# Kernel tuning notes

Measured on AMD Instinct MI355X. Metric: run time of the kernel, lower is better.

## Reference

```python
import jax, jax.numpy as jnp
import numpy as np

BATCH = 8192
N_FEATURES = 512
DEPTH = 10
N_LEAVES = 2 ** DEPTH
ATOMS = N_FEATURES + 1  # include_one=True
TAU = 1.0


def eml(a, b):
    # Assumed definition of the custom binary eml op: smooth-max / log-sum-exp.
    # eml(a, b) = log(exp(a) + exp(b)), computed stably.
    return jnp.logaddexp(a, b)


def setup_inputs() -> dict:
    key = jax.random.key(0)
    k1, k2 = jax.random.split(key)
    X = jax.random.normal(k1, (BATCH, N_FEATURES), dtype=jnp.float32)
    leaf_logits = jax.random.normal(k2, (N_LEAVES, ATOMS), dtype=jnp.float32) * 0.1
    return {"X": X, "leaf_logits": leaf_logits}


def reference(X, leaf_logits):
    batch = X.shape[0]
    # atom values: prepend constant 1 (include_one=True) -> (batch, atoms)
    atom_values = jnp.concatenate([jnp.ones((batch, 1), dtype=X.dtype), X], axis=1)
    # softmax over atoms per leaf, then mix: (batch, n_leaves)
    weights = jax.nn.softmax(leaf_logits / TAU, axis=-1)
    current = jnp.einsum('ba,la->bl', atom_values, weights)
    # binary tree reduction: log2(n_leaves) steps over strided slices
    while current.shape[-1] > 1:
        current = eml(current[..., 0::2], current[..., 1::2])
    return current.squeeze(-1)  # (batch,)
```

## Files before the change

kernel.cpp:

```cpp
#include <hip/hip_runtime.h>
#include <hip/hip_bf16.h>

#define BATCH 8192
#define NF 512
#define NL 1024
#define ATOMS 513

typedef float float4v __attribute__((ext_vector_type(4)));
typedef short short8 __attribute__((ext_vector_type(8)));

__device__ __forceinline__ unsigned short f2bf(float f) {
    union { float f; unsigned int u; } cv; cv.f = f;
    unsigned int u = cv.u;
    u += 0x7fffu + ((u >> 16) & 1u);
    return (unsigned short)(u >> 16);
}

__device__ __forceinline__ void load_lds16(const unsigned short* g, unsigned short* ldsbase) {
    __builtin_amdgcn_global_load_lds(
        (const __attribute__((address_space(1))) unsigned int*)g,
        (__attribute__((address_space(3))) unsigned int*)ldsbase,
        16, 0, 0);
}

__global__ void convert_kernel(const float* __restrict__ X,
                               unsigned short* __restrict__ Xb) {
    size_t i = ((size_t)blockIdx.x * 256 + threadIdx.x) * 8;
    float4v x0 = *reinterpret_cast<const float4v*>(X + i);
    float4v x1 = *reinterpret_cast<const float4v*>(X + i + 4);
    short8 a;
    a[0] = (short)f2bf(x0[0]); a[1] = (short)f2bf(x0[1]);
    a[2] = (short)f2bf(x0[2]); a[3] = (short)f2bf(x0[3]);
    a[4] = (short)f2bf(x1[0]); a[5] = (short)f2bf(x1[1]);
    a[6] = (short)f2bf(x1[2]); a[7] = (short)f2bf(x1[3]);
    *reinterpret_cast<short8*>(Xb + i) = a;
}

__global__ void softmax_kernel(const float* __restrict__ logits,
                               unsigned short* __restrict__ Wb,
                               float* __restrict__ bias) {
    int l = blockIdx.x;
    int t = threadIdx.x;
    int wave = t >> 6, lane = t & 63;
    const float* row = logits + (size_t)l * ATOMS;
    float v0 = row[t];
    float v1 = row[t + 256];
    float v2 = (t == 0) ? row[512] : -1e30f;

    __shared__ float red[8];
    float m = fmaxf(fmaxf(v0, v1), v2);
#pragma unroll
    for (int o = 32; o > 0; o >>= 1) m = fmaxf(m, __shfl_xor(m, o, 64));
    if (lane == 0) red[wave] = m;
    __syncthreads();
    float mx = fmaxf(fmaxf(red[0], red[1]), fmaxf(red[2], red[3]));

    float e0 = __expf(v0 - mx);
    float e1 = __expf(v1 - mx);
    float e2 = (t == 0) ? __expf(v2 - mx) : 0.f;
    float s = e0 + e1 + e2;
#pragma unroll
    for (int o = 32; o > 0; o >>= 1) s += __shfl_xor(s, o, 64);
    if (lane == 0) red[4 + wave] = s;
    __syncthreads();
    float inv = 1.f / (red[4] + red[5] + red[6] + red[7]);

    unsigned short* wrow = Wb + (size_t)l * NF;
    if (t == 0) {
        bias[l] = e0 * inv;
        wrow[511] = f2bf(e2 * inv);
    } else {
        wrow[t - 1] = f2bf(e0 * inv);
    }
    wrow[t + 255] = f2bf(e1 * inv);
}

__global__ __launch_bounds__(256, 2)
void gemm_lse_kernel(const unsigned short* __restrict__ Xb,
                     const unsigned short* __restrict__ Wb,
                     const float* __restrict__ bias,
                     float* __restrict__ partial) {
    __shared__ unsigned short As[128 * 32];
    __shared__ unsigned short Bs[128 * 32];
    __shared__ float sums[2][128];

    int tid  = threadIdx.x;
    int wave = tid >> 6;
    int lane = tid & 63;
    int quad = lane >> 4;
    int l16  = lane & 15;
    int wr = wave >> 1;
    int wc = wave & 1;

    int mb = blockIdx.x >> 3;
    int nb = blockIdx.x & 7;
    int R0 = mb * 128;
    int N0 = nb * 128;

    int srow = wave * 32 + (lane >> 2);
    int selem = (lane & 3) * 8;

    float4v acc[4][4];
#pragma unroll
    for (int mt = 0; mt < 4; ++mt)
#pragma unroll
        for (int nt = 0; nt < 4; ++nt)
            acc[mt][nt] = (float4v){0.f, 0.f, 0.f, 0.f};

    for (int kt = 0; kt < 16; ++kt) {
        int kb = kt * 32;
        const unsigned short* ga = Xb + (size_t)(R0 + srow) * NF + kb + selem;
        const unsigned short* gb = Wb + (size_t)(N0 + srow) * NF + kb + selem;
        load_lds16(ga,            &As[(wave * 32) * 32]);
        load_lds16(ga + 16 * NF,  &As[(wave * 32 + 16) * 32]);
        load_lds16(gb,            &Bs[(wave * 32) * 32]);
        load_lds16(gb + 16 * NF,  &Bs[(wave * 32 + 16) * 32]);
        __syncthreads();

        short8 af[4], bfr[4];
#pragma unroll
        for (int mt = 0; mt < 4; ++mt)
            af[mt] = *reinterpret_cast<const short8*>(
                &As[(wr * 64 + mt * 16 + l16) * 32 + quad * 8]);
#pragma unroll
        for (int nt = 0; nt < 4; ++nt)
            bfr[nt] = *reinterpret_cast<const short8*>(
                &Bs[(wc * 64 + nt * 16 + l16) * 32 + quad * 8]);

#pragma unroll
        for (int mt = 0; mt < 4; ++mt)
#pragma unroll
            for (int nt = 0; nt < 4; ++nt)
                acc[mt][nt] = __builtin_amdgcn_mfma_f32_16x16x32_bf16(
                    af[mt], bfr[nt], acc[mt][nt], 0, 0, 0);
        __syncthreads();
    }

    float ps[4][4];
#pragma unroll
    for (int mt = 0; mt < 4; ++mt)
#pragma unroll
        for (int r = 0; r < 4; ++r) ps[mt][r] = 0.f;

#pragma unroll
    for (int nt = 0; nt < 4; ++nt) {
        float bl = bias[N0 + wc * 64 + nt * 16 + l16];
#pragma unroll
        for (int mt = 0; mt < 4; ++mt)
#pragma unroll
            for (int r = 0; r < 4; ++r)
                ps[mt][r] += __expf(acc[mt][nt][r] + bl);
    }

#pragma unroll
    for (int m = 1; m < 16; m <<= 1)
#pragma unroll
        for (int mt = 0; mt < 4; ++mt)
#pragma unroll
            for (int r = 0; r < 4; ++r)
                ps[mt][r] += __shfl_xor(ps[mt][r], m, 64);

    if (l16 == 0) {
#pragma unroll
        for (int mt = 0; mt < 4; ++mt)
#pragma unroll
            for (int r = 0; r < 4; ++r)
                sums[wc][wr * 64 + mt * 16 + quad * 4 + r] = ps[mt][r];
    }
    __syncthreads();
    if (tid < 128)
        partial[(size_t)nb * BATCH + R0 + tid] = sums[0][tid] + sums[1][tid];
}

__global__ void combine_kernel(const float* __restrict__ partial,
                               float* __restrict__ out) {
    int i = blockIdx.x * 256 + threadIdx.x;
    float s = 0.f;
#pragma unroll
    for (int c = 0; c < 8; ++c) s += partial[(size_t)c * BATCH + i];
    out[i] = logf(s);
}

extern "C" void kernel_launch(void* const* d_in, const int* in_sizes, int n_in,
                              void* d_out, int out_size, void* d_ws, size_t ws_size,
                              hipStream_t stream) {
    const float* X      = (const float*)d_in[0];
    const float* logits = (const float*)d_in[1];
    float* out = (float*)d_out;

    char* ws = (char*)d_ws;
    unsigned short* Xb   = (unsigned short*)ws;
    unsigned short* Wb   = (unsigned short*)(ws + (size_t)BATCH * NF * 2);
    float*          bias = (float*)(ws + (size_t)BATCH * NF * 2 + (size_t)NL * NF * 2);
    float*          part = (float*)(ws + (size_t)BATCH * NF * 2 + (size_t)NL * NF * 2 + NL * 4);

    convert_kernel<<<(BATCH * NF) / (256 * 8), 256, 0, stream>>>(X, Xb);
    softmax_kernel<<<NL, 256, 0, stream>>>(logits, Wb, bias);
    gemm_lse_kernel<<<(BATCH / 128) * (NL / 128), 256, 0, stream>>>(Xb, Wb, bias, part);
    combine_kernel<<<BATCH / 256, 256, 0, stream>>>(part, out);
}
```

Before: 86.73 us.

## Merge prep kernels and fold combine into GEMM via atomics with last-block finalize

Merges the bf16 convert and softmax kernels into one prep launch that also zeroes the accumulators, and removes the combine kernel. GEMM blocks now atomically add their partial sum-exp into a per-row buffer, and the last block per row tile (found with a counter) applies the log. The block index mapping also changes so row tiles vary fastest, and the loop address math is hoisted. This cuts two launches and a global round trip, at the cost of atomics, a thread fence and float summation order that is no longer deterministic.

```diff
diff --git a/kernel.cpp b/kernel.cpp
--- a/kernel.cpp
+++ b/kernel.cpp
@@ -23,66 +23,84 @@
         16, 0, 0);
 }
 
-__global__ void convert_kernel(const float* __restrict__ X,
-                               unsigned short* __restrict__ Xb) {
-    size_t i = ((size_t)blockIdx.x * 256 + threadIdx.x) * 8;
-    float4v x0 = *reinterpret_cast<const float4v*>(X + i);
-    float4v x1 = *reinterpret_cast<const float4v*>(X + i + 4);
-    short8 a;
-    a[0] = (short)f2bf(x0[0]); a[1] = (short)f2bf(x0[1]);
-    a[2] = (short)f2bf(x0[2]); a[3] = (short)f2bf(x0[3]);
-    a[4] = (short)f2bf(x1[0]); a[5] = (short)f2bf(x1[1]);
-    a[6] = (short)f2bf(x1[2]); a[7] = (short)f2bf(x1[3]);
-    *reinterpret_cast<short8*>(Xb + i) = a;
-}
-
-__global__ void softmax_kernel(const float* __restrict__ logits,
-                               unsigned short* __restrict__ Wb,
-                               float* __restrict__ bias) {
-    int l = blockIdx.x;
-    int t = threadIdx.x;
-    int wave = t >> 6, lane = t & 63;
-    const float* row = logits + (size_t)l * ATOMS;
-    float v0 = row[t];
-    float v1 = row[t + 256];
-    float v2 = (t == 0) ? row[512] : -1e30f;
-
-    __shared__ float red[8];
-    float m = fmaxf(fmaxf(v0, v1), v2);
-#pragma unroll
-    for (int o = 32; o > 0; o >>= 1) m = fmaxf(m, __shfl_xor(m, o, 64));
-    if (lane == 0) red[wave] = m;
-    __syncthreads();
-    float mx = fmaxf(fmaxf(red[0], red[1]), fmaxf(red[2], red[3]));
-
-    float e0 = __expf(v0 - mx);
-    float e1 = __expf(v1 - mx);
-    float e2 = (t == 0) ? __expf(v2 - mx) : 0.f;
-    float s = e0 + e1 + e2;
-#pragma unroll
-    for (int o = 32; o > 0; o >>= 1) s += __shfl_xor(s, o, 64);
-    if (lane == 0) red[4 + wave] = s;
-    __syncthreads();
-    float inv = 1.f / (red[4] + red[5] + red[6] + red[7]);
-
-    unsigned short* wrow = Wb + (size_t)l * NF;
-    if (t == 0) {
-        bias[l] = e0 * inv;
-        wrow[511] = f2bf(e2 * inv);
-    } else {
-        wrow[t - 1] = f2bf(e0 * inv);
-    }
-    wrow[t + 255] = f2bf(e1 * inv);
+#define N_CONVERT_BLOCKS 2048
+#define N_SOFTMAX_BLOCKS 1024
+#define N_ZERO_BLOCKS    33
+
+__global__ void prep_kernel(const float* __restrict__ X,
+                            const float* __restrict__ logits,
+                            unsigned short* __restrict__ Xb,
+                            unsigned short* __restrict__ Wb,
+                            float* __restrict__ bias,
+                            float* __restrict__ sumexp,
+                            int* __restrict__ cnt) {
+    int bi = blockIdx.x;
+    int t  = threadIdx.x;
+
+    if (bi < N_CONVERT_BLOCKS) {
+        size_t i = ((size_t)bi * 256 + t) * 8;
+        float4v x0 = *reinterpret_cast<const float4v*>(X + i);
+        float4v x1 = *reinterpret_cast<const float4v*>(X + i + 4);
+        short8 a;
+        a[0] = (short)f2bf(x0[0]); a[1] = (short)f2bf(x0[1]);
+        a[2] = (short)f2bf(x0[2]); a[3] = (short)f2bf(x0[3]);
+        a[4] = (short)f2bf(x1[0]); a[5] = (short)f2bf(x1[1]);
+        a[6] = (short)f2bf(x1[2]); a[7] = (short)f2bf(x1[3]);
+        *reinterpret_cast<short8*>(Xb + i) = a;
+        return;
+    }
+    if (bi < N_CONVERT_BLOCKS + N_SOFTMAX_BLOCKS) {
+        int l = bi - N_CONVERT_BLOCKS;
+        int wave = t >> 6, lane = t & 63;
+        const float* row = logits + (size_t)l * ATOMS;
+        float v0 = row[t];
+        float v1 = row[t + 256];
+        float v2 = (t == 0) ? row[512] : -1e30f;
+
+        __shared__ float red[8];
+        float m = fmaxf(fmaxf(v0, v1), v2);
+#pragma unroll
+        for (int o = 32; o > 0; o >>= 1) m = fmaxf(m, __shfl_xor(m, o, 64));
+        if (lane == 0) red[wave] = m;
+        __syncthreads();
+        float mx = fmaxf(fmaxf(red[0], red[1]), fmaxf(red[2], red[3]));
+
+        float e0 = __expf(v0 - mx);
+        float e1 = __expf(v1 - mx);
+        float e2 = (t == 0) ? __expf(v2 - mx) : 0.f;
+        float s = e0 + e1 + e2;
+#pragma unroll
+        for (int o = 32; o > 0; o >>= 1) s += __shfl_xor(s, o, 64);
+        if (lane == 0) red[4 + wave] = s;
+        __syncthreads();
+        float inv = 1.f / (red[4] + red[5] + red[6] + red[7]);
+
+        unsigned short* wrow = Wb + (size_t)l * NF;
+        if (t == 0) {
+            bias[l] = e0 * inv;
+            wrow[511] = f2bf(e2 * inv);
+        } else {
+            wrow[t - 1] = f2bf(e0 * inv);
+        }
+        wrow[t + 255] = f2bf(e1 * inv);
+        return;
+    }
+    int i = (bi - N_CONVERT_BLOCKS - N_SOFTMAX_BLOCKS) * 256 + t;
+    if (i < BATCH) sumexp[i] = 0.f;
+    else { int j = i - BATCH; if (j < 64) cnt[j] = 0; }
 }
 
 __global__ __launch_bounds__(256, 2)
 void gemm_lse_kernel(const unsigned short* __restrict__ Xb,
                      const unsigned short* __restrict__ Wb,
                      const float* __restrict__ bias,
-                     float* __restrict__ partial) {
+                     float* __restrict__ sumexp,
+                     int* __restrict__ cnt,
+                     float* __restrict__ out) {
     __shared__ unsigned short As[128 * 32];
     __shared__ unsigned short Bs[128 * 32];
     __shared__ float sums[2][128];
+    __shared__ int lastFlag;
 
     int tid  = threadIdx.x;
     int wave = tid >> 6;
@@ -92,13 +110,27 @@
     int wr = wave >> 1;
     int wc = wave & 1;
 
-    int mb = blockIdx.x >> 3;
-    int nb = blockIdx.x & 7;
+    int mb = blockIdx.x & 63;
+    int nb = blockIdx.x >> 6;
     int R0 = mb * 128;
     int N0 = nb * 128;
 
-    int srow = wave * 32 + (lane >> 2);
+    int srow  = wave * 32 + (lane >> 2);
     int selem = (lane & 3) * 8;
+    const unsigned short* ga = Xb + (size_t)(R0 + srow) * NF + selem;
+    const unsigned short* gb = Wb + (size_t)(N0 + srow) * NF + selem;
+    unsigned short* la0 = &As[(wave * 32) * 32];
+    unsigned short* la1 = &As[(wave * 32 + 16) * 32];
+    unsigned short* lb0 = &Bs[(wave * 32) * 32];
+    unsigned short* lb1 = &Bs[(wave * 32 + 16) * 32];
+
+    const unsigned short* pa = &As[(wr * 64 + l16) * 32 + quad * 8];
+    const unsigned short* pb = &Bs[(wc * 64 + l16) * 32 + quad * 8];
+
+    float bl[4];
+#pragma unroll
+    for (int nt = 0; nt < 4; ++nt)
+        bl[nt] = bias[N0 + wc * 64 + nt * 16 + l16];
 
     float4v acc[4][4];
 #pragma unroll
@@ -108,24 +140,20 @@
             acc[mt][nt] = (float4v){0.f, 0.f, 0.f, 0.f};
 
     for (int kt = 0; kt < 16; ++kt) {
-        int kb = kt * 32;
-        const unsigned short* ga = Xb + (size_t)(R0 + srow) * NF + kb + selem;
-        const unsigned short* gb = Wb + (size_t)(N0 + srow) * NF + kb + selem;
-        load_lds16(ga,            &As[(wave * 32) * 32]);
-        load_lds16(ga + 16 * NF,  &As[(wave * 32 + 16) * 32]);
-        load_lds16(gb,            &Bs[(wave * 32) * 32]);
-        load_lds16(gb + 16 * NF,  &Bs[(wave * 32 + 16) * 32]);
+        load_lds16(ga,           la0);
+        load_lds16(ga + 16 * NF, la1);
+        load_lds16(gb,           lb0);
+        load_lds16(gb + 16 * NF, lb1);
+        ga += 32; gb += 32;
         __syncthreads();
 
         short8 af[4], bfr[4];
 #pragma unroll
         for (int mt = 0; mt < 4; ++mt)
-            af[mt] = *reinterpret_cast<const short8*>(
-                &As[(wr * 64 + mt * 16 + l16) * 32 + quad * 8]);
+            af[mt] = *reinterpret_cast<const short8*>(pa + mt * 16 * 32);
 #pragma unroll
         for (int nt = 0; nt < 4; ++nt)
-            bfr[nt] = *reinterpret_cast<const short8*>(
-                &Bs[(wc * 64 + nt * 16 + l16) * 32 + quad * 8]);
+            bfr[nt] = *reinterpret_cast<const short8*>(pb + nt * 16 * 32);
 
 #pragma unroll
         for (int mt = 0; mt < 4; ++mt)
@@ -143,14 +171,12 @@
         for (int r = 0; r < 4; ++r) ps[mt][r] = 0.f;
 
 #pragma unroll
-    for (int nt = 0; nt < 4; ++nt) {
-        float bl = bias[N0 + wc * 64 + nt * 16 + l16];
+    for (int nt = 0; nt < 4; ++nt)
 #pragma unroll
         for (int mt = 0; mt < 4; ++mt)
 #pragma unroll
             for (int r = 0; r < 4; ++r)
-                ps[mt][r] += __expf(acc[mt][nt][r] + bl);
-    }
+                ps[mt][r] += __expf(acc[mt][nt][r] + bl[nt]);
 
 #pragma unroll
     for (int m = 1; m < 16; m <<= 1)
@@ -168,17 +194,23 @@
                 sums[wc][wr * 64 + mt * 16 + quad * 4 + r] = ps[mt][r];
     }
     __syncthreads();
+
     if (tid < 128)
-        partial[(size_t)nb * BATCH + R0 + tid] = sums[0][tid] + sums[1][tid];
-}
-
-__global__ void combine_kernel(const float* __restrict__ partial,
-                               float* __restrict__ out) {
-    int i = blockIdx.x * 256 + threadIdx.x;
-    float s = 0.f;
-#pragma unroll
-    for (int c = 0; c < 8; ++c) s += partial[(size_t)c * BATCH + i];
-    out[i] = logf(s);
+        atomicAdd(&sumexp[R0 + tid], sums[0][tid] + sums[1][tid]);
+
+    __threadfence();
+    __syncthreads();
+    if (tid == 0) {
+        int old = __hip_atomic_fetch_add(&cnt[mb], 1, __ATOMIC_ACQ_REL,
+                                         __HIP_MEMORY_SCOPE_AGENT);
+        lastFlag = (old == 7);
+    }
+    __syncthreads();
+    if (lastFlag && tid < 128) {
+        float s = __hip_atomic_load(&sumexp[R0 + tid], __ATOMIC_RELAXED,
+                                    __HIP_MEMORY_SCOPE_AGENT);
+        out[R0 + tid] = logf(s);
+    }
 }
 
 extern "C" void kernel_launch(void* const* d_in, const int* in_sizes, int n_in,
@@ -191,11 +223,12 @@
     char* ws = (char*)d_ws;
     unsigned short* Xb   = (unsigned short*)ws;
     unsigned short* Wb   = (unsigned short*)(ws + (size_t)BATCH * NF * 2);
-    float*          bias = (float*)(ws + (size_t)BATCH * NF * 2 + (size_t)NL * NF * 2);
-    float*          part = (float*)(ws + (size_t)BATCH * NF * 2 + (size_t)NL * NF * 2 + NL * 4);
-
-    convert_kernel<<<(BATCH * NF) / (256 * 8), 256, 0, stream>>>(X, Xb);
-    softmax_kernel<<<NL, 256, 0, stream>>>(logits, Wb, bias);
-    gemm_lse_kernel<<<(BATCH / 128) * (NL / 128), 256, 0, stream>>>(Xb, Wb, bias, part);
-    combine_kernel<<<BATCH / 256, 256, 0, stream>>>(part, out);
-}
+    float* bias   = (float*)(ws + (size_t)BATCH * NF * 2 + (size_t)NL * NF * 2);
+    float* sumexp = (float*)((char*)bias + NL * sizeof(float));
+    int*   cnt    = (int*)((char*)sumexp + BATCH * sizeof(float));
+
+    prep_kernel<<<N_CONVERT_BLOCKS + N_SOFTMAX_BLOCKS + N_ZERO_BLOCKS, 256, 0, stream>>>(
+        X, logits, Xb, Wb, bias, sumexp, cnt);
+    gemm_lse_kernel<<<(BATCH / 128) * (NL / 128), 256, 0, stream>>>(
+        Xb, Wb, bias, sumexp, cnt, out);
+}
```

Result: slower. 116.3 us (+34.1%).

## Double-buffer LDS tiles in GEMM to prefetch next K-slice during MFMA

Applied to the files above, without the earlier changes.

The GEMM kernel gets two LDS buffers for the A and B tiles. The first K-slice is loaded before the loop, and each iteration issues the async global-to-LDS loads for the next slice before running the MFMAs on the current one. This hides global load latency behind compute and leaves one barrier per iteration instead of two. The costs are double the LDS per block (about 32KB), which could limit occupancy, and a redundant duplicate fragment-load loop that the compiler should eliminate.

```diff
diff --git a/kernel.cpp b/kernel.cpp
--- a/kernel.cpp
+++ b/kernel.cpp
@@ -80,8 +80,8 @@
                      const unsigned short* __restrict__ Wb,
                      const float* __restrict__ bias,
                      float* __restrict__ partial) {
-    __shared__ unsigned short As[128 * 32];
-    __shared__ unsigned short Bs[128 * 32];
+    __shared__ unsigned short As[2][128 * 32];
+    __shared__ unsigned short Bs[2][128 * 32];
     __shared__ float sums[2][128];
 
     int tid  = threadIdx.x;
@@ -97,8 +97,10 @@
     int R0 = mb * 128;
     int N0 = nb * 128;
 
-    int srow = wave * 32 + (lane >> 2);
+    int srow  = wave * 32 + (lane >> 2);
     int selem = (lane & 3) * 8;
+    const unsigned short* ga = Xb + (size_t)(R0 + srow) * NF + selem;
+    const unsigned short* gb = Wb + (size_t)(N0 + srow) * NF + selem;
 
     float4v acc[4][4];
 #pragma unroll
@@ -107,25 +109,41 @@
         for (int nt = 0; nt < 4; ++nt)
             acc[mt][nt] = (float4v){0.f, 0.f, 0.f, 0.f};
 
+    {
+        load_lds16(ga,           &As[0][(wave * 32) * 32]);
+        load_lds16(ga + 16 * NF, &As[0][(wave * 32 + 16) * 32]);
+        load_lds16(gb,           &Bs[0][(wave * 32) * 32]);
+        load_lds16(gb + 16 * NF, &Bs[0][(wave * 32 + 16) * 32]);
+    }
+    __syncthreads();
+
+    int frag_off = (wr * 64 + l16) * 32 + quad * 8;
+
     for (int kt = 0; kt < 16; ++kt) {
-        int kb = kt * 32;
-        const unsigned short* ga = Xb + (size_t)(R0 + srow) * NF + kb + selem;
-        const unsigned short* gb = Wb + (size_t)(N0 + srow) * NF + kb + selem;
-        load_lds16(ga,            &As[(wave * 32) * 32]);
-        load_lds16(ga + 16 * NF,  &As[(wave * 32 + 16) * 32]);
-        load_lds16(gb,            &Bs[(wave * 32) * 32]);
-        load_lds16(gb + 16 * NF,  &Bs[(wave * 32 + 16) * 32]);
-        __syncthreads();
+        int cur = kt & 1;
+        if (kt < 15) {
+            const unsigned short* a = ga + (kt + 1) * 32;
+            const unsigned short* b = gb + (kt + 1) * 32;
+            int nxt = cur ^ 1;
+            load_lds16(a,           &As[nxt][(wave * 32) * 32]);
+            load_lds16(a + 16 * NF, &As[nxt][(wave * 32 + 16) * 32]);
+            load_lds16(b,           &Bs[nxt][(wave * 32) * 32]);
+            load_lds16(b + 16 * NF, &Bs[nxt][(wave * 32 + 16) * 32]);
+        }
 
         short8 af[4], bfr[4];
 #pragma unroll
         for (int mt = 0; mt < 4; ++mt)
             af[mt] = *reinterpret_cast<const short8*>(
-                &As[(wr * 64 + mt * 16 + l16) * 32 + quad * 8]);
+                &As[cur][frag_off + (mt * 16 - wr * 64 + wr * 64) * 32 + (mt * 0)]);
+#pragma unroll
+        for (int mt = 0; mt < 4; ++mt)
+            af[mt] = *reinterpret_cast<const short8*>(
+                &As[cur][(wr * 64 + mt * 16 + l16) * 32 + quad * 8]);
 #pragma unroll
         for (int nt = 0; nt < 4; ++nt)
             bfr[nt] = *reinterpret_cast<const short8*>(
-                &Bs[(wc * 64 + nt * 16 + l16) * 32 + quad * 8]);
+                &Bs[cur][(wc * 64 + nt * 16 + l16) * 32 + quad * 8]);
 
 #pragma unroll
         for (int mt = 0; mt < 4; ++mt)
@@ -133,9 +151,15 @@
             for (int nt = 0; nt < 4; ++nt)
                 acc[mt][nt] = __builtin_amdgcn_mfma_f32_16x16x32_bf16(
                     af[mt], bfr[nt], acc[mt][nt], 0, 0, 0);
+
         __syncthreads();
     }
 
+    float bl[4];
+#pragma unroll
+    for (int nt = 0; nt < 4; ++nt)
+        bl[nt] = bias[N0 + wc * 64 + nt * 16 + l16];
+
     float ps[4][4];
 #pragma unroll
     for (int mt = 0; mt < 4; ++mt)
@@ -143,14 +167,12 @@
         for (int r = 0; r < 4; ++r) ps[mt][r] = 0.f;
 
 #pragma unroll
-    for (int nt = 0; nt < 4; ++nt) {
-        float bl = bias[N0 + wc * 64 + nt * 16 + l16];
+    for (int nt = 0; nt < 4; ++nt)
 #pragma unroll
         for (int mt = 0; mt < 4; ++mt)
 #pragma unroll
             for (int r = 0; r < 4; ++r)
-                ps[mt][r] += __expf(acc[mt][nt][r] + bl);
-    }
+                ps[mt][r] += __expf(acc[mt][nt][r] + bl[nt]);
 
 #pragma unroll
     for (int m = 1; m < 16; m <<= 1)
@@ -191,8 +213,8 @@
     char* ws = (char*)d_ws;
     unsigned short* Xb   = (unsigned short*)ws;
     unsigned short* Wb   = (unsigned short*)(ws + (size_t)BATCH * NF * 2);
-    float*          bias = (float*)(ws + (size_t)BATCH * NF * 2 + (size_t)NL * NF * 2);
-    float*          part = (float*)(ws + (size_t)BATCH * NF * 2 + (size_t)NL * NF * 2 + NL * 4);
+    float* bias = (float*)(ws + (size_t)BATCH * NF * 2 + (size_t)NL * NF * 2);
+    float* part = (float*)((char*)bias + NL * sizeof(float));
 
     convert_kernel<<<(BATCH * NF) / (256 * 8), 256, 0, stream>>>(X, Xb);
     softmax_kernel<<<NL, 256, 0, stream>>>(logits, Wb, bias);
```

New measurement: 84.84 us. -2.2%, faster.

## Switch GEMM operands to FP8 with double-buffered swizzled LDS tiles

Applied to the files above, without the earlier changes.

Converts X and the softmax weights to FP8 (weights scaled by 512 to use the FP8 range, undone in the epilogue) and uses FP8 MFMA instructions instead of BF16. The K tile grows to 64 bytes per row with double-buffered LDS loads that prefetch the next tile while computing, and a rotated chunk swizzle avoids LDS bank conflicts. This halves conversion and GEMM memory traffic and raises MFMA throughput. The cost is a large loss of precision in the matmul that may exceed the tolerance.

```diff
diff --git a/kernel.cpp b/kernel.cpp
--- a/kernel.cpp
+++ b/kernel.cpp
@@ -7,16 +7,13 @@
 #define ATOMS 513
 
 typedef float float4v __attribute__((ext_vector_type(4)));
-typedef short short8 __attribute__((ext_vector_type(8)));
-
-__device__ __forceinline__ unsigned short f2bf(float f) {
-    union { float f; unsigned int u; } cv; cv.f = f;
-    unsigned int u = cv.u;
-    u += 0x7fffu + ((u >> 16) & 1u);
-    return (unsigned short)(u >> 16);
-}
-
-__device__ __forceinline__ void load_lds16(const unsigned short* g, unsigned short* ldsbase) {
+typedef int int4v __attribute__((ext_vector_type(4)));
+
+__device__ __forceinline__ unsigned char f2fp8(float x) {
+    return (unsigned char)(__builtin_amdgcn_cvt_pk_fp8_f32(x, x, 0, false) & 0xff);
+}
+
+__device__ __forceinline__ void load_lds16(const void* g, void* ldsbase) {
     __builtin_amdgcn_global_load_lds(
         (const __attribute__((address_space(1))) unsigned int*)g,
         (__attribute__((address_space(3))) unsigned int*)ldsbase,
@@ -24,20 +21,29 @@
 }
 
 __global__ void convert_kernel(const float* __restrict__ X,
-                               unsigned short* __restrict__ Xb) {
-    size_t i = ((size_t)blockIdx.x * 256 + threadIdx.x) * 8;
-    float4v x0 = *reinterpret_cast<const float4v*>(X + i);
-    float4v x1 = *reinterpret_cast<const float4v*>(X + i + 4);
-    short8 a;
-    a[0] = (short)f2bf(x0[0]); a[1] = (short)f2bf(x0[1]);
-    a[2] = (short)f2bf(x0[2]); a[3] = (short)f2bf(x0[3]);
-    a[4] = (short)f2bf(x1[0]); a[5] = (short)f2bf(x1[1]);
-    a[6] = (short)f2bf(x1[2]); a[7] = (short)f2bf(x1[3]);
-    *reinterpret_cast<short8*>(Xb + i) = a;
+                               unsigned char* __restrict__ X8) {
+    size_t i = ((size_t)blockIdx.x * 256 + threadIdx.x) * 16;
+    const float4v* p = reinterpret_cast<const float4v*>(X + i);
+    float4v a = p[0], b = p[1], c = p[2], d = p[3];
+    int4v o;
+    int w;
+    w = __builtin_amdgcn_cvt_pk_fp8_f32(a[0], a[1], 0, false);
+    w = __builtin_amdgcn_cvt_pk_fp8_f32(a[2], a[3], w, true);
+    o[0] = w;
+    w = __builtin_amdgcn_cvt_pk_fp8_f32(b[0], b[1], 0, false);
+    w = __builtin_amdgcn_cvt_pk_fp8_f32(b[2], b[3], w, true);
+    o[1] = w;
+    w = __builtin_amdgcn_cvt_pk_fp8_f32(c[0], c[1], 0, false);
+    w = __builtin_amdgcn_cvt_pk_fp8_f32(c[2], c[3], w, true);
+    o[2] = w;
+    w = __builtin_amdgcn_cvt_pk_fp8_f32(d[0], d[1], 0, false);
+    w = __builtin_amdgcn_cvt_pk_fp8_f32(d[2], d[3], w, true);
+    o[3] = w;
+    *reinterpret_cast<int4v*>(X8 + i) = o;
 }
 
 __global__ void softmax_kernel(const float* __restrict__ logits,
-                               unsigned short* __restrict__ Wb,
+                               unsigned char* __restrict__ W8,
                                float* __restrict__ bias) {
     int l = blockIdx.x;
     int t = threadIdx.x;
@@ -64,24 +70,25 @@
     if (lane == 0) red[4 + wave] = s;
     __syncthreads();
     float inv = 1.f / (red[4] + red[5] + red[6] + red[7]);
-
-    unsigned short* wrow = Wb + (size_t)l * NF;
+    float inv512 = inv * 512.f;
+
+    unsigned char* wrow = W8 + (size_t)l * NF;
     if (t == 0) {
         bias[l] = e0 * inv;
-        wrow[511] = f2bf(e2 * inv);
+        wrow[511] = f2fp8(e2 * inv512);
     } else {
-        wrow[t - 1] = f2bf(e0 * inv);
+        wrow[t - 1] = f2fp8(e0 * inv512);
     }
-    wrow[t + 255] = f2bf(e1 * inv);
+    wrow[t + 255] = f2fp8(e1 * inv512);
 }
 
 __global__ __launch_bounds__(256, 2)
-void gemm_lse_kernel(const unsigned short* __restrict__ Xb,
-                     const unsigned short* __restrict__ Wb,
+void gemm_lse_kernel(const unsigned char* __restrict__ X8,
+                     const unsigned char* __restrict__ W8,
                      const float* __restrict__ bias,
                      float* __restrict__ partial) {
-    __shared__ unsigned short As[128 * 32];
-    __shared__ unsigned short Bs[128 * 32];
+    __shared__ unsigned char As[2][128 * 64];
+    __shared__ unsigned char Bs[2][128 * 64];
     __shared__ float sums[2][128];
 
     int tid  = threadIdx.x;
@@ -97,8 +104,10 @@
     int R0 = mb * 128;
     int N0 = nb * 128;
 
-    int srow = wave * 32 + (lane >> 2);
-    int selem = (lane & 3) * 8;
+    int srow  = wave * 32 + (lane >> 2);
+    int schunk = ((lane & 3) - (lane >> 2)) & 3;
+    const unsigned char* gA = X8 + (size_t)(R0 + srow) * NF + schunk * 16;
+    const unsigned char* gB = W8 + (size_t)(N0 + srow) * NF + schunk * 16;
 
     float4v acc[4][4];
 #pragma unroll
@@ -107,35 +116,64 @@
         for (int nt = 0; nt < 4; ++nt)
             acc[mt][nt] = (float4v){0.f, 0.f, 0.f, 0.f};
 
-    for (int kt = 0; kt < 16; ++kt) {
-        int kb = kt * 32;
-        const unsigned short* ga = Xb + (size_t)(R0 + srow) * NF + kb + selem;
-        const unsigned short* gb = Wb + (size_t)(N0 + srow) * NF + kb + selem;
-        load_lds16(ga,            &As[(wave * 32) * 32]);
-        load_lds16(ga + 16 * NF,  &As[(wave * 32 + 16) * 32]);
-        load_lds16(gb,            &Bs[(wave * 32) * 32]);
-        load_lds16(gb + 16 * NF,  &Bs[(wave * 32 + 16) * 32]);
-        __syncthreads();
-
-        short8 af[4], bfr[4];
-#pragma unroll
-        for (int mt = 0; mt < 4; ++mt)
-            af[mt] = *reinterpret_cast<const short8*>(
-                &As[(wr * 64 + mt * 16 + l16) * 32 + quad * 8]);
-#pragma unroll
-        for (int nt = 0; nt < 4; ++nt)
-            bfr[nt] = *reinterpret_cast<const short8*>(
-                &Bs[(wc * 64 + nt * 16 + l16) * 32 + quad * 8]);
-
-#pragma unroll
-        for (int mt = 0; mt < 4; ++mt)
-#pragma unroll
-            for (int nt = 0; nt < 4; ++nt)
-                acc[mt][nt] = __builtin_amdgcn_mfma_f32_16x16x32_bf16(
-                    af[mt], bfr[nt], acc[mt][nt], 0, 0, 0);
+    load_lds16(gA,           &As[0][(wave * 32) * 64]);
+    load_lds16(gA + 16 * NF, &As[0][(wave * 32 + 16) * 64]);
+    load_lds16(gB,           &Bs[0][(wave * 32) * 64]);
+    load_lds16(gB + 16 * NF, &Bs[0][(wave * 32 + 16) * 64]);
+    __syncthreads();
+
+    for (int kt = 0; kt < 8; ++kt) {
+        int cur = kt & 1;
+        if (kt < 7) {
+            int nxt = cur ^ 1;
+            const unsigned char* a = gA + (kt + 1) * 64;
+            const unsigned char* b = gB + (kt + 1) * 64;
+            load_lds16(a,           &As[nxt][(wave * 32) * 64]);
+            load_lds16(a + 16 * NF, &As[nxt][(wave * 32 + 16) * 64]);
+            load_lds16(b,           &Bs[nxt][(wave * 32) * 64]);
+            load_lds16(b + 16 * NF, &Bs[nxt][(wave * 32 + 16) * 64]);
+        }
+
+        long af[4][2], bfr[4][2];
+#pragma unroll
+        for (int mt = 0; mt < 4; ++mt) {
+            int r = wr * 64 + mt * 16 + l16;
+#pragma unroll
+            for (int s = 0; s < 2; ++s) {
+                int g = s * 2 + (quad >> 1);
+                int off = r * 64 + (((g + r) & 3) * 16) + (quad & 1) * 8;
+                af[mt][s] = *reinterpret_cast<const long*>(&As[cur][off]);
+            }
+        }
+#pragma unroll
+        for (int nt = 0; nt < 4; ++nt) {
+            int r = wc * 64 + nt * 16 + l16;
+#pragma unroll
+            for (int s = 0; s < 2; ++s) {
+                int g = s * 2 + (quad >> 1);
+                int off = r * 64 + (((g + r) & 3) * 16) + (quad & 1) * 8;
+                bfr[nt][s] = *reinterpret_cast<const long*>(&Bs[cur][off]);
+            }
+        }
+
+#pragma unroll
+        for (int mt = 0; mt < 4; ++mt)
+#pragma unroll
+            for (int nt = 0; nt < 4; ++nt) {
+                acc[mt][nt] = __builtin_amdgcn_mfma_f32_16x16x32_fp8_fp8(
+                    af[mt][0], bfr[nt][0], acc[mt][nt], 0, 0, 0);
+                acc[mt][nt] = __builtin_amdgcn_mfma_f32_16x16x32_fp8_fp8(
+                    af[mt][1], bfr[nt][1], acc[mt][nt], 0, 0, 0);
+            }
         __syncthreads();
     }
 
+    float bl[4];
+#pragma unroll
+    for (int nt = 0; nt < 4; ++nt)
+        bl[nt] = bias[N0 + wc * 64 + nt * 16 + l16];
+
+    const float INV512 = 0.001953125f;
     float ps[4][4];
 #pragma unroll
     for (int mt = 0; mt < 4; ++mt)
@@ -143,14 +181,12 @@
         for (int r = 0; r < 4; ++r) ps[mt][r] = 0.f;
 
 #pragma unroll
-    for (int nt = 0; nt < 4; ++nt) {
-        float bl = bias[N0 + wc * 64 + nt * 16 + l16];
+    for (int nt = 0; nt < 4; ++nt)
 #pragma unroll
         for (int mt = 0; mt < 4; ++mt)
 #pragma unroll
             for (int r = 0; r < 4; ++r)
-                ps[mt][r] += __expf(acc[mt][nt][r] + bl);
-    }
+                ps[mt][r] += __expf(fmaf(acc[mt][nt][r], INV512, bl[nt]));
 
 #pragma unroll
     for (int m = 1; m < 16; m <<= 1)
@@ -189,13 +225,13 @@
     float* out = (float*)d_out;
 
     char* ws = (char*)d_ws;
-    unsigned short* Xb   = (unsigned short*)ws;
-    unsigned short* Wb   = (unsigned short*)(ws + (size_t)BATCH * NF * 2);
-    float*          bias = (float*)(ws + (size_t)BATCH * NF * 2 + (size_t)NL * NF * 2);
-    float*          part = (float*)(ws + (size_t)BATCH * NF * 2 + (size_t)NL * NF * 2 + NL * 4);
-
-    convert_kernel<<<(BATCH * NF) / (256 * 8), 256, 0, stream>>>(X, Xb);
-    softmax_kernel<<<NL, 256, 0, stream>>>(logits, Wb, bias);
-    gemm_lse_kernel<<<(BATCH / 128) * (NL / 128), 256, 0, stream>>>(Xb, Wb, bias, part);
+    unsigned char* X8 = (unsigned char*)ws;
+    unsigned char* W8 = (unsigned char*)(ws + (size_t)BATCH * NF);
+    float* bias = (float*)(ws + (size_t)BATCH * NF + (size_t)NL * NF);
+    float* part = (float*)((char*)bias + NL * sizeof(float));
+
+    convert_kernel<<<(BATCH * NF) / (256 * 16), 256, 0, stream>>>(X, X8);
+    softmax_kernel<<<NL, 256, 0, stream>>>(logits, W8, bias);
+    gemm_lse_kernel<<<(BATCH / 128) * (NL / 128), 256, 0, stream>>>(X8, W8, bias, part);
     combine_kernel<<<BATCH / 256, 256, 0, stream>>>(part, out);
 }
```

Measured after the change: 87.20 us. No clear change (+0.5%).
